# Optimization experiments

Hardware: AMD Instinct MI355X
Metric: run time of the kernel (lower is better)

Reference implementation:

```python
import jax, jax.numpy as jnp
import numpy as np

OUT = 2048          # rows of sparse weight (out_features)
IN = 2048           # cols of sparse weight (in_features)
NNZ_PER_ROW = 128   # uniform nnz per row -> simple valid CSR indptr
NNZ = OUT * NNZ_PER_ROW
N = 512             # number of input rows (tokens)


def setup_inputs() -> dict:
    key = jax.random.key(0)
    k1, k2, k3 = jax.random.split(key, 3)
    x = jax.random.normal(k1, (N, IN), dtype=jnp.float32)
    data = jax.random.normal(k2, (NNZ,), dtype=jnp.float32)
    # sorted column indices per row (canonical-ish CSR; duplicates are harmless, they sum)
    indices = jnp.sort(
        jax.random.randint(k3, (OUT, NNZ_PER_ROW), 0, IN), axis=1
    ).reshape(NNZ).astype(jnp.int32)
    indptr = (jnp.arange(OUT + 1) * NNZ_PER_ROW).astype(jnp.int32)
    return {"x": x, "data": data, "indices": indices, "indptr": indptr}


def reference(x, data, indices, indptr):
    # CuPyLinear.forward: result = (W_csr @ x.T).T, i.e. y = x @ W.T with W sparse CSR.
    nnz = data.shape[0]
    n_rows = indptr.shape[0] - 1  # static
    # expand CSR indptr to per-nnz row ids
    rows = jnp.searchsorted(indptr, jnp.arange(nnz, dtype=indptr.dtype), side="right") - 1
    # contrib[k, n] = data[k] * x[n, col[k]]
    contrib = data[:, None] * x.T[indices]                 # [nnz, N]
    y_t = jax.ops.segment_sum(contrib, rows, num_segments=n_rows)  # [out, N]
    return y_t.T                                           # [N, out]
```

## Files before the change

kernel.cpp:

```cpp
#include <hip/hip_runtime.h>

#define N_TOK 512
#define IN_F  2048
#define OUT_F 2048
#define NNZ_ROW 128

#define ROW_G 4
#define TOK_G 256

__device__ ushort g_xT16[IN_F * N_TOK];

static __device__ __forceinline__ ushort f2bf(float f) {
    unsigned u = __float_as_uint(f);
    unsigned r = (u + 0x7fffu + ((u >> 16) & 1u)) >> 16;
    return (ushort)r;
}

__global__ __launch_bounds__(256) void transpose_x(const float* __restrict__ x) {
    __shared__ float tile[32][33];
    const int bx = blockIdx.x;
    const int by = blockIdx.y;
    const int tx = threadIdx.x;
    const int ty = threadIdx.y;

    const int col  = bx * 32 + tx;
    const int row0 = by * 32 + ty;
#pragma unroll
    for (int j = 0; j < 32; j += 8)
        tile[ty + j][tx] = x[(row0 + j) * IN_F + col];
    __syncthreads();

    const int n  = by * 32 + tx;
    const int c0 = bx * 32 + ty;
#pragma unroll
    for (int j = 0; j < 32; j += 8)
        g_xT16[(c0 + j) * N_TOK + n] = f2bf(tile[tx][ty + j]);
}

__global__ __launch_bounds__(256) void spmm_csr(const float* __restrict__ data,
                                                const int*   __restrict__ indices,
                                                const int*   __restrict__ indptr,
                                                float*       __restrict__ y) {
    const int rg = blockIdx.x;
    const int tg = blockIdx.y;
    const int r0 = rg * ROW_G;
    const int t  = threadIdx.x;

    __shared__ int2  s_wi[ROW_G * NNZ_ROW];
    __shared__ float ytile[ROW_G][TOK_G + 4];

#pragma unroll
    for (int i = 0; i < 2; ++i) {
        const int g    = t + i * 256;
        const int rl   = g >> 7;
        const int off  = g & (NNZ_ROW - 1);
        const int base = indptr[r0 + rl] + off;
        s_wi[g] = make_int2(indices[base] * (N_TOK / 4), __float_as_int(data[base]));
    }
    __syncthreads();

    const uint2* __restrict__ xT2 = (const uint2*)g_xT16;
    const int w = t >> 6;
    const int l = t & 63;
    const int tokoff = tg * (TOK_G / 4) + l;

    const int2* __restrict__ p = &s_wi[w * NNZ_ROW];
    float4 acc = make_float4(0.f, 0.f, 0.f, 0.f);
#pragma unroll 16
    for (int k = 0; k < NNZ_ROW; ++k) {
        const int2 wi  = p[k];
        const int  off = __builtin_amdgcn_readfirstlane(wi.x);
        const float wt = __int_as_float(__builtin_amdgcn_readfirstlane(wi.y));
        const uint2 u  = xT2[off + tokoff];
        acc.x += wt * __uint_as_float(u.x << 16);
        acc.y += wt * __uint_as_float(u.x);
        acc.z += wt * __uint_as_float(u.y << 16);
        acc.w += wt * __uint_as_float(u.y);
    }
    *(float4*)&ytile[w][4 * l] = acc;
    __syncthreads();

    const int n0 = tg * TOK_G;
#pragma unroll
    for (int i = 0; i < 4; ++i) {
        const int g = t + i * 256;
        const int n = g >> 2;
        const int f = g & (ROW_G - 1);
        y[(n0 + n) * OUT_F + r0 + f] = ytile[f][n];
    }
}

extern "C" void kernel_launch(void* const* d_in, const int* in_sizes, int n_in,
                              void* d_out, int out_size, void* d_ws, size_t ws_size,
                              hipStream_t stream) {
    const float* x       = (const float*)d_in[0];
    const float* data    = (const float*)d_in[1];
    const int*   indices = (const int*)  d_in[2];
    const int*   indptr  = (const int*)  d_in[3];
    float*       y       = (float*)d_out;

    dim3 tb(32, 8);
    dim3 tg(IN_F / 32, N_TOK / 32);
    transpose_x<<<tg, tb, 0, stream>>>(x);

    dim3 sg(OUT_F / ROW_G, N_TOK / TOK_G);
    spmm_csr<<<sg, 256, 0, stream>>>(data, indices, indptr, y);
}
```

Before: 81.50 us.

## Densify sparse weights and run fp16 MFMA dense GEMM instead of CSR SpMM

```diff
diff --git a/kernel.cpp b/kernel.cpp
--- a/kernel.cpp
+++ b/kernel.cpp
@@ -1,93 +1,144 @@
 #include <hip/hip_runtime.h>
+#include <hip/hip_fp16.h>
 
 #define N_TOK 512
 #define IN_F  2048
 #define OUT_F 2048
 #define NNZ_ROW 128
 
-#define ROW_G 4
-#define TOK_G 256
+#define BM 64
+#define BN 64
+#define BK 64
+#define KT (IN_F / BK)
 
-__device__ ushort g_xT16[IN_F * N_TOK];
+typedef __attribute__((ext_vector_type(8))) _Float16 f16x8;
+typedef __attribute__((ext_vector_type(4))) float    f32x4;
 
-static __device__ __forceinline__ ushort f2bf(float f) {
-    unsigned u = __float_as_uint(f);
-    unsigned r = (u + 0x7fffu + ((u >> 16) & 1u)) >> 16;
-    return (ushort)r;
+__device__ __half g_xA[N_TOK * IN_F];
+__device__ __half g_Wd[OUT_F * IN_F];
+
+__global__ __launch_bounds__(256) void pack_x(const float* __restrict__ x) {
+    const int i = blockIdx.x * 256 + threadIdx.x;
+    const float4 v = ((const float4*)x)[i];
+    __half2* o = (__half2*)g_xA;
+    o[2 * i + 0] = __floats2half2_rn(v.x, v.y);
+    o[2 * i + 1] = __floats2half2_rn(v.z, v.w);
 }
 
-__global__ __launch_bounds__(256) void transpose_x(const float* __restrict__ x) {
-    __shared__ float tile[32][33];
-    const int bx = blockIdx.x;
-    const int by = blockIdx.y;
-    const int tx = threadIdx.x;
-    const int ty = threadIdx.y;
+#define DR 4
+__global__ __launch_bounds__(256) void densify(const float* __restrict__ data,
+                                               const int*   __restrict__ indices,
+                                               const int*   __restrict__ indptr) {
+    __shared__ float s_acc[DR][IN_F];
+    const int r0 = blockIdx.x * DR;
+    const int t  = threadIdx.x;
 
-    const int col  = bx * 32 + tx;
-    const int row0 = by * 32 + ty;
 #pragma unroll
-    for (int j = 0; j < 32; j += 8)
-        tile[ty + j][tx] = x[(row0 + j) * IN_F + col];
+    for (int i = 0; i < (DR * IN_F) / (256 * 4); ++i)
+        ((float4*)&s_acc[0][0])[t + i * 256] = make_float4(0.f, 0.f, 0.f, 0.f);
     __syncthreads();
 
-    const int n  = by * 32 + tx;
-    const int c0 = bx * 32 + ty;
 #pragma unroll
-    for (int j = 0; j < 32; j += 8)
-        g_xT16[(c0 + j) * N_TOK + n] = f2bf(tile[tx][ty + j]);
-}
-
-__global__ __launch_bounds__(256) void spmm_csr(const float* __restrict__ data,
-                                                const int*   __restrict__ indices,
-                                                const int*   __restrict__ indptr,
-                                                float*       __restrict__ y) {
-    const int rg = blockIdx.x;
-    const int tg = blockIdx.y;
-    const int r0 = rg * ROW_G;
-    const int t  = threadIdx.x;
-
-    __shared__ int2  s_wi[ROW_G * NNZ_ROW];
-    __shared__ float ytile[ROW_G][TOK_G + 4];
-
-#pragma unroll
-    for (int i = 0; i < 2; ++i) {
-        const int g    = t + i * 256;
-        const int rl   = g >> 7;
-        const int off  = g & (NNZ_ROW - 1);
-        const int base = indptr[r0 + rl] + off;
-        s_wi[g] = make_int2(indices[base] * (N_TOK / 4), __float_as_int(data[base]));
+    for (int i = 0; i < (DR * NNZ_ROW) / 256; ++i) {
+        const int g  = t + i * 256;
+        const int rl = g >> 7;
+        const int k  = indptr[r0 + rl] + (g & (NNZ_ROW - 1));
+        atomicAdd(&s_acc[rl][indices[k]], data[k]);
     }
     __syncthreads();
 
-    const uint2* __restrict__ xT2 = (const uint2*)g_xT16;
-    const int w = t >> 6;
-    const int l = t & 63;
-    const int tokoff = tg * (TOK_G / 4) + l;
+#pragma unroll
+    for (int i = 0; i < (DR * IN_F) / (256 * 2); ++i) {
+        const int g  = t + i * 256;
+        const int rl = g >> 10;
+        const int c2 = g & 1023;
+        ((__half2*)&g_Wd[(size_t)(r0 + rl) * IN_F])[c2] =
+            __floats2half2_rn(s_acc[rl][2 * c2], s_acc[rl][2 * c2 + 1]);
+    }
+}
 
-    const int2* __restrict__ p = &s_wi[w * NNZ_ROW];
-    float4 acc = make_float4(0.f, 0.f, 0.f, 0.f);
-#pragma unroll 16
-    for (int k = 0; k < NNZ_ROW; ++k) {
-        const int2 wi  = p[k];
-        const int  off = __builtin_amdgcn_readfirstlane(wi.x);
-        const float wt = __int_as_float(__builtin_amdgcn_readfirstlane(wi.y));
-        const uint2 u  = xT2[off + tokoff];
-        acc.x += wt * __uint_as_float(u.x << 16);
-        acc.y += wt * __uint_as_float(u.x);
-        acc.z += wt * __uint_as_float(u.y << 16);
-        acc.w += wt * __uint_as_float(u.y);
+__global__ __launch_bounds__(256) void gemm_f16(float* __restrict__ y) {
+    const int nt = blockIdx.x;
+    const int mt = blockIdx.y;
+    const int m0 = mt * BM, n0 = nt * BN;
+    const int t  = threadIdx.x;
+    const int w  = t >> 6, l = t & 63;
+    const int fr = l & 15, fq = l >> 4;
+    const int wm = w >> 1, wn = w & 1;
+
+    __shared__ __half Ab[2][BM * BK];
+    __shared__ __half Bb[2][BN * BK];
+
+    const char* Ag = (const char*)g_xA + (size_t)m0 * (IN_F * 2);
+    const char* Bg = (const char*)g_Wd + (size_t)n0 * (IN_F * 2);
+
+    auto STAGE = [&](int buf, int kt_) {
+        const int kbb = kt_ * (BK * 2);
+#pragma unroll
+        for (int j = 0; j < 2; ++j) {
+            const int off = (t + j * 256) * 16;
+            const int row = off >> 7;
+            const int scb = (off & 127) ^ ((row & 7) << 4);
+            __builtin_amdgcn_global_load_lds(
+                (const unsigned*)(Ag + row * (IN_F * 2) + kbb + scb),
+                (unsigned*)((char*)&Ab[buf][0] + off), 16, 0, 0);
+            __builtin_amdgcn_global_load_lds(
+                (const unsigned*)(Bg + row * (IN_F * 2) + kbb + scb),
+                (unsigned*)((char*)&Bb[buf][0] + off), 16, 0, 0);
+        }
+    };
+
+    int aoff[2][2], boff[2][2];
+#pragma unroll
+    for (int r = 0; r < 2; ++r)
+#pragma unroll
+        for (int ks = 0; ks < 2; ++ks) {
+            const int cb = (ks * 64 + fq * 16) ^ ((fr & 7) << 4);
+            aoff[r][ks] = (wm * 32 + r * 16 + fr) * 128 + cb;
+            boff[r][ks] = (wn * 32 + r * 16 + fr) * 128 + cb;
+        }
+
+    f32x4 acc[2][2];
+#pragma unroll
+    for (int i = 0; i < 2; ++i)
+#pragma unroll
+        for (int j = 0; j < 2; ++j)
+            acc[i][j] = (f32x4){0.f, 0.f, 0.f, 0.f};
+
+    STAGE(0, 0);
+    __syncthreads();
+    int cur = 0;
+    for (int kt = 0; kt < KT; ++kt) {
+        if (kt + 1 < KT) STAGE(cur ^ 1, kt + 1);
+        f16x8 a[2][2], b[2][2];
+#pragma unroll
+        for (int r = 0; r < 2; ++r)
+#pragma unroll
+            for (int ks = 0; ks < 2; ++ks) {
+                a[r][ks] = *(const f16x8*)((const char*)&Ab[cur][0] + aoff[r][ks]);
+                b[r][ks] = *(const f16x8*)((const char*)&Bb[cur][0] + boff[r][ks]);
+            }
+#pragma unroll
+        for (int mr = 0; mr < 2; ++mr)
+#pragma unroll
+            for (int nr = 0; nr < 2; ++nr)
+#pragma unroll
+                for (int ks = 0; ks < 2; ++ks)
+                    acc[mr][nr] = __builtin_amdgcn_mfma_f32_16x16x32_f16(
+                        a[mr][ks], b[nr][ks], acc[mr][nr], 0, 0, 0);
+        __syncthreads();
+        cur ^= 1;
     }
-    *(float4*)&ytile[w][4 * l] = acc;
-    __syncthreads();
 
-    const int n0 = tg * TOK_G;
+    float* yb = y + (size_t)m0 * OUT_F + n0;
 #pragma unroll
-    for (int i = 0; i < 4; ++i) {
-        const int g = t + i * 256;
-        const int n = g >> 2;
-        const int f = g & (ROW_G - 1);
-        y[(n0 + n) * OUT_F + r0 + f] = ytile[f][n];
-    }
+    for (int mr = 0; mr < 2; ++mr)
+#pragma unroll
+        for (int nr = 0; nr < 2; ++nr)
+#pragma unroll
+            for (int j = 0; j < 4; ++j)
+                yb[(size_t)(wm * 32 + mr * 16 + fq * 4 + j) * OUT_F +
+                   (wn * 32 + nr * 16 + fr)] = acc[mr][nr][j];
 }
 
 extern "C" void kernel_launch(void* const* d_in, const int* in_sizes, int n_in,
@@ -99,10 +150,7 @@
     const int*   indptr  = (const int*)  d_in[3];
     float*       y       = (float*)d_out;
 
-    dim3 tb(32, 8);
-    dim3 tg(IN_F / 32, N_TOK / 32);
-    transpose_x<<<tg, tb, 0, stream>>>(x);
-
-    dim3 sg(OUT_F / ROW_G, N_TOK / TOK_G);
-    spmm_csr<<<sg, 256, 0, stream>>>(data, indices, indptr, y);
+    pack_x<<<dim3((N_TOK * IN_F) / (4 * 256)), 256, 0, stream>>>(x);
+    densify<<<dim3(OUT_F / DR), 256, 0, stream>>>(data, indices, indptr);
+    gemm_f16<<<dim3(OUT_F / BN, N_TOK / BM), 256, 0, stream>>>(y);
 }
```

New measurement: 96.92 us. +18.9%, slower.

## Tile x into LDS token blocks and pack weight+index into one word

Applied to the files above, without the earlier changes.

```diff
diff --git a/kernel.cpp b/kernel.cpp
--- a/kernel.cpp
+++ b/kernel.cpp
@@ -5,89 +5,119 @@
 #define OUT_F 2048
 #define NNZ_ROW 128
 
-#define ROW_G 4
-#define TOK_G 256
+#define TTOK 8
+#define NTILE (N_TOK / TTOK)
 
-__device__ ushort g_xT16[IN_F * N_TOK];
+#define ROWS 64
+#define TPB  32
+#define TILES_PB (TPB / TTOK)
+#define WPITCH 132
+#define YPITCH 36
 
-static __device__ __forceinline__ ushort f2bf(float f) {
+#define SW_BYTES (ROWS * WPITCH * 4)
+#define SX_BYTES (IN_F * TTOK * 2)
+#define SY_BYTES (ROWS * YPITCH * 4)
+#define SMEM_BYTES (SW_BYTES + SX_BYTES + SY_BYTES)
+
+__device__ ushort g_xt[NTILE * IN_F * TTOK];
+
+static __device__ __forceinline__ unsigned f2bf(float f) {
     unsigned u = __float_as_uint(f);
-    unsigned r = (u + 0x7fffu + ((u >> 16) & 1u)) >> 16;
-    return (ushort)r;
+    return (u + 0x7fffu + ((u >> 16) & 1u)) >> 16;
 }
 
-__global__ __launch_bounds__(256) void transpose_x(const float* __restrict__ x) {
-    __shared__ float tile[32][33];
-    const int bx = blockIdx.x;
-    const int by = blockIdx.y;
-    const int tx = threadIdx.x;
-    const int ty = threadIdx.y;
-
-    const int col  = bx * 32 + tx;
-    const int row0 = by * 32 + ty;
+__global__ __launch_bounds__(256) void tile_x(const float* __restrict__ x) {
+    const int tile = blockIdx.y;
+    const int c    = blockIdx.x * 256 + threadIdx.x;
+    unsigned o[4];
 #pragma unroll
-    for (int j = 0; j < 32; j += 8)
-        tile[ty + j][tx] = x[(row0 + j) * IN_F + col];
-    __syncthreads();
-
-    const int n  = by * 32 + tx;
-    const int c0 = bx * 32 + ty;
-#pragma unroll
-    for (int j = 0; j < 32; j += 8)
-        g_xT16[(c0 + j) * N_TOK + n] = f2bf(tile[tx][ty + j]);
+    for (int j = 0; j < 4; ++j) {
+        const float a = x[(tile * TTOK + 2 * j    ) * IN_F + c];
+        const float b = x[(tile * TTOK + 2 * j + 1) * IN_F + c];
+        o[j] = f2bf(a) | (f2bf(b) << 16);
+    }
+    ((uint4*)g_xt)[tile * IN_F + c] = make_uint4(o[0], o[1], o[2], o[3]);
 }
 
-__global__ __launch_bounds__(256) void spmm_csr(const float* __restrict__ data,
-                                                const int*   __restrict__ indices,
-                                                const int*   __restrict__ indptr,
-                                                float*       __restrict__ y) {
+__global__ __launch_bounds__(256, 2) void spmm(const float* __restrict__ data,
+                                               const int*   __restrict__ indices,
+                                               const int*   __restrict__ indptr,
+                                               float*       __restrict__ y) {
+    extern __shared__ unsigned smem[];
+    unsigned* s_w = smem;
+    ushort*   s_x = (ushort*)((char*)smem + SW_BYTES);
+    float*    s_y = (float*)((char*)smem + SW_BYTES + SX_BYTES);
+
     const int rg = blockIdx.x;
-    const int tg = blockIdx.y;
-    const int r0 = rg * ROW_G;
+    const int tb = blockIdx.y;
+    const int r0 = rg * ROWS;
     const int t  = threadIdx.x;
 
-    __shared__ int2  s_wi[ROW_G * NNZ_ROW];
-    __shared__ float ytile[ROW_G][TOK_G + 4];
+    const int base0 = indptr[r0];
+    const int4*   I4 = (const int4*)(indices + base0);
+    const float4* D4 = (const float4*)(data + base0);
+#pragma unroll
+    for (int i = 0; i < (ROWS * NNZ_ROW / 4) / 256; ++i) {
+        const int    e  = t + i * 256;
+        const int4   ci = I4[e];
+        const float4 dv = D4[e];
+        const int    r  = e >> 5;
+        const int    k0 = (e & 31) * 4;
+        unsigned* dst = &s_w[r * WPITCH + k0];
+        dst[0] = (__float_as_uint(dv.x) & 0xFFFFF800u) | (unsigned)ci.x;
+        dst[1] = (__float_as_uint(dv.y) & 0xFFFFF800u) | (unsigned)ci.y;
+        dst[2] = (__float_as_uint(dv.z) & 0xFFFFF800u) | (unsigned)ci.z;
+        dst[3] = (__float_as_uint(dv.w) & 0xFFFFF800u) | (unsigned)ci.w;
+    }
 
+    const int l  = t & 63;
+    const int w  = t >> 6;
+    const int rw = w * 16 + (l >> 2);
+    const int q  = (l >> 1) & 1;
+    const int kh = l & 1;
+    const unsigned* wrow = &s_w[rw * WPITCH];
+    const uint2* sx2 = (const uint2*)s_x;
+
+    for (int ti = 0; ti < TILES_PB; ++ti) {
+        const char* src = (const char*)g_xt +
+                          (size_t)(tb * TILES_PB + ti) * SX_BYTES;
 #pragma unroll
-    for (int i = 0; i < 2; ++i) {
-        const int g    = t + i * 256;
-        const int rl   = g >> 7;
-        const int off  = g & (NNZ_ROW - 1);
-        const int base = indptr[r0 + rl] + off;
-        s_wi[g] = make_int2(indices[base] * (N_TOK / 4), __float_as_int(data[base]));
+        for (int i = 0; i < (SX_BYTES / 16) / 256; ++i) {
+            const int off = (t + i * 256) * 16;
+            __builtin_amdgcn_global_load_lds((const unsigned*)(src + off),
+                                             (unsigned*)((char*)s_x + off),
+                                             16, 0, 0);
+        }
+        __syncthreads();
+
+        float4 acc = make_float4(0.f, 0.f, 0.f, 0.f);
+#pragma unroll 8
+        for (int j = 0; j < NNZ_ROW / 2; ++j) {
+            const unsigned u  = wrow[2 * j + kh];
+            const float    wt = __uint_as_float(u & 0xFFFFF800u);
+            const uint2    xv = sx2[(u & 2047u) * 2 + q];
+            acc.x += wt * __uint_as_float(xv.x << 16);
+            acc.y += wt * __uint_as_float(xv.x);
+            acc.z += wt * __uint_as_float(xv.y << 16);
+            acc.w += wt * __uint_as_float(xv.y);
+        }
+        acc.x += __shfl_xor(acc.x, 1);
+        acc.y += __shfl_xor(acc.y, 1);
+        acc.z += __shfl_xor(acc.z, 1);
+        acc.w += __shfl_xor(acc.w, 1);
+        if (kh == 0)
+            *(float4*)&s_y[rw * YPITCH + ti * TTOK + q * 4] = acc;
+        __syncthreads();
     }
-    __syncthreads();
 
-    const uint2* __restrict__ xT2 = (const uint2*)g_xT16;
-    const int w = t >> 6;
-    const int l = t & 63;
-    const int tokoff = tg * (TOK_G / 4) + l;
-
-    const int2* __restrict__ p = &s_wi[w * NNZ_ROW];
-    float4 acc = make_float4(0.f, 0.f, 0.f, 0.f);
-#pragma unroll 16
-    for (int k = 0; k < NNZ_ROW; ++k) {
-        const int2 wi  = p[k];
-        const int  off = __builtin_amdgcn_readfirstlane(wi.x);
-        const float wt = __int_as_float(__builtin_amdgcn_readfirstlane(wi.y));
-        const uint2 u  = xT2[off + tokoff];
-        acc.x += wt * __uint_as_float(u.x << 16);
-        acc.y += wt * __uint_as_float(u.x);
-        acc.z += wt * __uint_as_float(u.y << 16);
-        acc.w += wt * __uint_as_float(u.y);
-    }
-    *(float4*)&ytile[w][4 * l] = acc;
-    __syncthreads();
-
-    const int n0 = tg * TOK_G;
+    const int n  = t >> 3;
+    const int rb = t & 7;
+    float v[8];
 #pragma unroll
-    for (int i = 0; i < 4; ++i) {
-        const int g = t + i * 256;
-        const int n = g >> 2;
-        const int f = g & (ROW_G - 1);
-        y[(n0 + n) * OUT_F + r0 + f] = ytile[f][n];
-    }
+    for (int j = 0; j < 8; ++j) v[j] = s_y[(rb * 8 + j) * YPITCH + n];
+    float* yp = &y[(size_t)(tb * TPB + n) * OUT_F + r0 + rb * 8];
+    *(float4*)yp       = make_float4(v[0], v[1], v[2], v[3]);
+    *((float4*)yp + 1) = make_float4(v[4], v[5], v[6], v[7]);
 }
 
 extern "C" void kernel_launch(void* const* d_in, const int* in_sizes, int n_in,
@@ -99,10 +129,7 @@
     const int*   indptr  = (const int*)  d_in[3];
     float*       y       = (float*)d_out;
 
-    dim3 tb(32, 8);
-    dim3 tg(IN_F / 32, N_TOK / 32);
-    transpose_x<<<tg, tb, 0, stream>>>(x);
-
-    dim3 sg(OUT_F / ROW_G, N_TOK / TOK_G);
-    spmm_csr<<<sg, 256, 0, stream>>>(data, indices, indptr, y);
+    tile_x<<<dim3(IN_F / 256, NTILE), 256, 0, stream>>>(x);
+    spmm<<<dim3(OUT_F / ROWS, N_TOK / TPB), 256, SMEM_BYTES, stream>>>(
+        data, indices, indptr, y);
 }
```

New measurement: 79.41 us. 1.03x faster.
